# Kernel optimization log

Measured on AMD Instinct MI355X. Metric: run time of the kernel, lower is better.

The kernel has to match this reference:

```python
import jax, jax.numpy as jnp
import numpy as np

T, B, N, D, H = 128, 64, 24, 256, 8
F = D // H  # 32


def setup_inputs() -> dict:
    key = jax.random.key(0)
    ks = jax.random.split(key, 7)
    s = 1.0 / np.sqrt(D)  # torch nn.Linear default init range
    inputs = jax.random.normal(ks[0], (T, B, N * D), dtype=jnp.float32)
    Wk = jax.random.uniform(ks[1], (H, F, D), minval=-s, maxval=s, dtype=jnp.float32)
    bk = jax.random.uniform(ks[2], (H, F), minval=-s, maxval=s, dtype=jnp.float32)
    Wv = jax.random.uniform(ks[3], (H, F, D), minval=-s, maxval=s, dtype=jnp.float32)
    bv = jax.random.uniform(ks[4], (H, F), minval=-s, maxval=s, dtype=jnp.float32)
    Wq = jax.random.uniform(ks[5], (H, N, F, D), minval=-s, maxval=s, dtype=jnp.float32)
    bq = jax.random.uniform(ks[6], (H, N, F), minval=-s, maxval=s, dtype=jnp.float32)
    return {"inputs": inputs, "Wk": Wk, "bk": bk, "Wv": Wv, "bv": bv, "Wq": Wq, "bq": bq}


def reference(inputs, Wk, bk, Wv, bv, Wq, bq):
    # inputs: (T, B, N*D) -> (T, B, N, D)
    x = inputs.reshape(T, B, N, D)
    # shared K/V per head: (T, B, H, N, F)
    k = jnp.einsum('tbnd,hfd->tbhnf', x, Wk) + bk[:, None, :]
    v = jnp.einsum('tbnd,hfd->tbhnf', x, Wv) + bv[:, None, :]
    # per-joint Q: joint n uses its own (F, D) weight -> (T, B, H, N, F)
    q = jnp.einsum('tbnd,hnfd->tbhnf', x, Wq) + bq
    # attention over joints, scaled by sqrt(F)
    scores = jnp.einsum('tbhnf,tbhmf->tbhnm', q, k) / jnp.sqrt(jnp.float32(F))
    attn = jax.nn.softmax(scores, axis=-1)
    out = jnp.einsum('tbhnm,tbhmf->tbhnf', attn, v)
    # concat heads along feature dim per joint, then flatten joints: (T, B, N*H*F)
    out = out.transpose(0, 1, 3, 2, 4).reshape(T, B, N * H * F)
    # dropout is identity in eval mode
    return out
```

## Files before the change

### kernel.cpp

```cpp
#include <hip/hip_runtime.h>
#include <hip/hip_bf16.h>
#include <cstdio>

#define TB  8192
#define N_  24
#define D_  256
#define H_  8
#define F_  32
#define ND  6144
#define HNF 6144

typedef unsigned short u16;
typedef __attribute__((ext_vector_type(8))) _Float16 f16x8;
typedef __attribute__((ext_vector_type(8))) short bf16x8;
typedef __attribute__((ext_vector_type(4))) float f32x4;

__device__ __forceinline__ u16 f2b(float f) {
    unsigned int u = __float_as_uint(f);
    return (u16)((u + 0x7FFFu + ((u >> 16) & 1u)) >> 16);
}
__device__ __forceinline__ float b2f(u16 s) {
    return __uint_as_float(((unsigned int)s) << 16);
}
__device__ __forceinline__ u16 f2h(float f) {
    _Float16 h = (_Float16)f;
    u16 u; __builtin_memcpy(&u, &h, 2); return u;
}

__device__ __forceinline__ void gl_lds16(const void* g, void* l) {
    __builtin_amdgcn_global_load_lds(
        (const __attribute__((address_space(1))) unsigned int*)g,
        (__attribute__((address_space(3))) unsigned int*)l, 16, 0, 0);
}

__global__ __launch_bounds__(256) void prep_weights(
    const float* __restrict__ Wk, const float* __restrict__ Wv,
    const float* __restrict__ Wq, u16* __restrict__ Bp)
{
    const int idx = blockIdx.x * 256 + threadIdx.x;
    if (idx >= 24 * 8 * 48 * 64) return;
    const int fr = idx & 15;
    const int fq = (idx >> 4) & 3;
    const int g  = (idx >> 6) % 48;
    const int kt = (idx / (64 * 48)) % 8;
    const int n  = idx / (64 * 48 * 8);
    const int col = g * 16 + fr;
    const int d0  = kt * 32 + fq * 8;
    const int c   = col & 255;
    const float* src;
    if (col < 256)      src = Wk + (size_t)c * 256 + d0;
    else if (col < 512) src = Wv + (size_t)c * 256 + d0;
    else {
        const int h = c >> 5, f = c & 31;
        src = Wq + ((size_t)(h * 24 + n) * 32 + f) * 256 + d0;
    }
    __align__(16) u16 out[8];
    #pragma unroll
    for (int j = 0; j < 8; ++j) out[j] = f2h(src[j]);
    *reinterpret_cast<uint4*>(Bp + (size_t)idx * 8) =
        *reinterpret_cast<const uint4*>(out);
}

__global__ __launch_bounds__(256) void prep_bias(
    const float* __restrict__ bk, const float* __restrict__ bv,
    const float* __restrict__ bq, float* __restrict__ biasp)
{
    const int idx = blockIdx.x * 256 + threadIdx.x;
    if (idx >= 24 * 768) return;
    const int col = idx % 768, n = idx / 768;
    const int c = col & 255;
    float v;
    if (col < 256)      v = bk[c];
    else if (col < 512) v = bv[c];
    else { const int h = c >> 5, f = c & 31; v = bq[(h * 24 + n) * 32 + f]; }
    biasp[n * 768 + col] = v;
}

__global__ __launch_bounds__(512, 4) void proj_mfma(
    const float* __restrict__ x,
    const u16* __restrict__ Bp,
    const float* __restrict__ biasp,
    u16* __restrict__ kb, u16* __restrict__ vb, u16* __restrict__ qb)
{
    const int lin  = blockIdx.x;
    const int mblk = lin & 63;
    const int ct   = (lin >> 6) % 3;
    const int n    = lin / 192;
    const int tb0  = mblk * 128;
    const int tid  = threadIdx.x;
    const int w    = tid >> 6;
    const int lane = tid & 63;
    const int wm   = w >> 2;
    const int wn   = w & 3;
    const int fr   = lane & 15, fq = lane >> 4;

    __shared__ __align__(16) u16 smem[32768];
    char* const Ab = (char*)smem;
    char* const Bb = (char*)smem + 16384;

    const int arow = tid >> 2;
    const int ac   = tid & 3;
    const float* xsrc = x + (size_t)(tb0 + arow) * ND + n * 256 + ac * 8;
    const int awbyte = arow * 64 + ((ac ^ ((arow >> 1) & 3)) << 4);

    const size_t bbase = (size_t)(n * 8 * 48 + ct * 16 + w * 2) * 1024 + lane * 16;

    f32x4 acc[4][4];
    #pragma unroll
    for (int m = 0; m < 4; ++m)
        #pragma unroll
        for (int j = 0; j < 4; ++j) acc[m][j] = (f32x4){0.f, 0.f, 0.f, 0.f};

    float4 axr[2][2];

    axr[0][0] = *reinterpret_cast<const float4*>(xsrc);
    axr[0][1] = *reinterpret_cast<const float4*>(xsrc + 4);
    gl_lds16((const char*)Bp + bbase,        Bb + (w * 2) * 1024);
    gl_lds16((const char*)Bp + bbase + 1024, Bb + (w * 2 + 1) * 1024);
    asm volatile("s_waitcnt vmcnt(2)" ::: "memory");
    {
        ushort4 hv;
        hv.x = f2h(axr[0][0].x); hv.y = f2h(axr[0][0].y);
        hv.z = f2h(axr[0][0].z); hv.w = f2h(axr[0][0].w);
        ushort4 hv2;
        hv2.x = f2h(axr[0][1].x); hv2.y = f2h(axr[0][1].y);
        hv2.z = f2h(axr[0][1].z); hv2.w = f2h(axr[0][1].w);
        *reinterpret_cast<ushort4*>(Ab + awbyte)     = hv;
        *reinterpret_cast<ushort4*>(Ab + awbyte + 8) = hv2;
    }
    axr[1][0] = *reinterpret_cast<const float4*>(xsrc + 32);
    axr[1][1] = *reinterpret_cast<const float4*>(xsrc + 36);
    asm volatile("s_waitcnt lgkmcnt(0)" ::: "memory");
    asm volatile("s_waitcnt vmcnt(2)" ::: "memory");
    __builtin_amdgcn_s_barrier();
    asm volatile("" ::: "memory");

    #pragma unroll
    for (int kt = 0; kt < 8; ++kt) {
        const int c = kt & 1, o = c ^ 1;

        if (kt < 7) {
            const size_t bs = bbase + (size_t)(kt + 1) * 48 * 1024;
            gl_lds16((const char*)Bp + bs,        Bb + o * 16384 + (w * 2) * 1024);
            gl_lds16((const char*)Bp + bs + 1024, Bb + o * 16384 + (w * 2 + 1) * 1024);
        }

        f16x8 bfr[4], afr[4];
        #pragma unroll
        for (int j = 0; j < 4; ++j)
            bfr[j] = *reinterpret_cast<const f16x8*>(
                Bb + c * 16384 + (wn * 4 + j) * 1024 + lane * 16);
        #pragma unroll
        for (int m = 0; m < 4; ++m) {
            const int row = wm * 64 + m * 16 + fr;
            afr[m] = *reinterpret_cast<const f16x8*>(
                Ab + c * 8192 + row * 64 + ((fq ^ ((fr >> 1) & 3)) << 4));
        }
        __builtin_amdgcn_s_setprio(1);
        #pragma unroll
        for (int j = 0; j < 4; ++j)
            #pragma unroll
            for (int m = 0; m < 4; ++m)
                acc[m][j] = __builtin_amdgcn_mfma_f32_16x16x32_f16(
                    afr[m], bfr[j], acc[m][j], 0, 0, 0);
        __builtin_amdgcn_s_setprio(0);

        if (kt < 7) {
            asm volatile("s_waitcnt vmcnt(2)" ::: "memory");
            __builtin_amdgcn_sched_barrier(0);
            {
                const float4 lo = axr[(kt + 1) & 1][0];
                const float4 hi = axr[(kt + 1) & 1][1];
                ushort4 hv;
                hv.x = f2h(lo.x); hv.y = f2h(lo.y); hv.z = f2h(lo.z); hv.w = f2h(lo.w);
                ushort4 hv2;
                hv2.x = f2h(hi.x); hv2.y = f2h(hi.y); hv2.z = f2h(hi.z); hv2.w = f2h(hi.w);
                *reinterpret_cast<ushort4*>(Ab + o * 8192 + awbyte)     = hv;
                *reinterpret_cast<ushort4*>(Ab + o * 8192 + awbyte + 8) = hv2;
            }
            if (kt < 6) {
                axr[kt & 1][0] = *reinterpret_cast<const float4*>(xsrc + (kt + 2) * 32);
                axr[kt & 1][1] = *reinterpret_cast<const float4*>(xsrc + (kt + 2) * 32 + 4);
            }
            asm volatile("s_waitcnt lgkmcnt(0)" ::: "memory");
            if (kt < 6) {
                asm volatile("s_waitcnt vmcnt(2)" ::: "memory");
            } else {
                asm volatile("s_waitcnt vmcnt(0)" ::: "memory");
            }
            __builtin_amdgcn_s_barrier();
            asm volatile("" ::: "memory");
        }
    }
    __syncthreads();

    #pragma unroll
    for (int j = 0; j < 4; ++j) {
        const int colL = wn * 64 + j * 16 + fr;
        const float bs = biasp[n * 768 + ct * 256 + colL];
        #pragma unroll
        for (int m = 0; m < 4; ++m)
            #pragma unroll
            for (int r = 0; r < 4; ++r) {
                const int rowL = wm * 64 + m * 16 + fq * 4 + r;
                const int byte = (rowL * 512 + colL * 2) ^ ((rowL & 7) << 4);
                *reinterpret_cast<u16*>((char*)smem + byte) = f2b(acc[m][j][r] + bs);
            }
    }
    __syncthreads();

    u16* dst = (ct == 0) ? kb : (ct == 1) ? vb : qb;
    #pragma unroll
    for (int it = 0; it < 8; ++it) {
        const int id  = it * 512 + tid;
        const int row = id >> 5;
        const int cch = id & 31;
        const uint4 v = *reinterpret_cast<const uint4*>(
            (char*)smem + (row * 512 + ((cch * 16) ^ ((row & 7) << 4))));
        const int cc = cch * 8;
        const int h  = cc >> 5, f0 = cc & 31;
        *reinterpret_cast<uint4*>(
            &dst[(size_t)(tb0 + row) * HNF + h * 768 + n * 32 + f0]) = v;
    }
}

__device__ __forceinline__ int swz(int row, int chunk) {
    return row * 32 + (((chunk ^ ((row >> 1) ^ (row >> 3))) & 3) << 3);
}

__global__ __launch_bounds__(256) void attn_mfma(
    const u16* __restrict__ kb,
    const u16* __restrict__ vb,
    const u16* __restrict__ qb,
    float* __restrict__ out)
{
    const int tid  = threadIdx.x;
    const int wid  = tid >> 6;
    const int lane = tid & 63;
    const int fr   = lane & 15;
    const int fq   = lane >> 4;
    const size_t tb = (size_t)blockIdx.x * 4 + wid;

    __shared__ __align__(16) u16 lds[4][2048];
    u16* Pw = lds[wid];
    u16* Vt = lds[wid] + 1024;

    #pragma unroll
    for (int i = 0; i < 4; ++i)
        reinterpret_cast<uint4*>(lds[wid])[lane + i * 64] = (uint4){0, 0, 0, 0};

    const u16* qt = qb + tb * HNF;
    const u16* kt = kb + tb * HNF;
    const u16* vt = vb + tb * HNF;
    float* outp = out + tb * ND;

    const float scale = 0.17677669529663687f;
    const bool colok = fr < 8;

    for (int h = 0; h < H_; ++h) {
        const u16* qh = qt + h * 768;
        const u16* kh = kt + h * 768;
        const u16* vh = vt + h * 768;

        bf16x8 qa[2], ka[2];
        #pragma unroll
        for (int t = 0; t < 2; ++t) {
            int rq = t * 16 + fr; rq = rq < 24 ? rq : 23;
            qa[t] = *reinterpret_cast<const bf16x8*>(qh + rq * 32 + fq * 8);
            ka[t] = *reinterpret_cast<const bf16x8*>(kh + rq * 32 + fq * 8);
        }

        {
            const int m = lane >> 2, q = lane & 3;
            const uint4 vv = *reinterpret_cast<const uint4*>(vh + m * 32 + q * 8);
            #pragma unroll
            for (int j = 0; j < 8; ++j) {
                const int f = q * 8 + j;
                Vt[swz(f, m >> 3) + (m & 7)] = reinterpret_cast<const u16*>(&vv)[j];
            }
            if (lane < 32) {
                const int m2 = 16 + (lane >> 2), q2 = lane & 3;
                const uint4 v2 = *reinterpret_cast<const uint4*>(vh + m2 * 32 + q2 * 8);
                #pragma unroll
                for (int j = 0; j < 8; ++j) {
                    const int f = q2 * 8 + j;
                    Vt[swz(f, m2 >> 3) + (m2 & 7)] = reinterpret_cast<const u16*>(&v2)[j];
                }
            }
        }

        f32x4 S[2][2];
        #pragma unroll
        for (int a = 0; a < 2; ++a)
            #pragma unroll
            for (int b = 0; b < 2; ++b)
                S[a][b] = __builtin_amdgcn_mfma_f32_16x16x32_bf16(
                    qa[a], ka[b], (f32x4){0.f, 0.f, 0.f, 0.f}, 0, 0, 0);

        float inv[2][4];
        #pragma unroll
        for (int t = 0; t < 2; ++t) {
            float e0[4], e1[4];
            #pragma unroll
            for (int r = 0; r < 4; ++r) {
                const float a = S[t][0][r] * scale;
                const float b = colok ? S[t][1][r] * scale : -1e30f;
                float mx = fmaxf(a, b);
                #pragma unroll
                for (int off = 1; off < 16; off <<= 1)
                    mx = fmaxf(mx, __shfl_xor(mx, off));
                e0[r] = __expf(a - mx);
                e1[r] = colok ? __expf(b - mx) : 0.f;
                float sm = e0[r] + e1[r];
                #pragma unroll
                for (int off = 1; off < 16; off <<= 1)
                    sm += __shfl_xor(sm, off);
                inv[t][r] = 1.f / sm;
            }
            #pragma unroll
            for (int r = 0; r < 4; ++r) {
                const int row = t * 16 + fq * 4 + r;
                if (row < 24) {
                    Pw[swz(row, fr >> 3) + (fr & 7)] = f2b(e0[r]);
                    if (colok) {
                        const int c1 = 16 + fr;
                        Pw[swz(row, c1 >> 3) + (c1 & 7)] = f2b(e1[r]);
                    }
                }
            }
        }

        bf16x8 pa[2], vbf[2];
        #pragma unroll
        for (int t = 0; t < 2; ++t)
            pa[t] = *reinterpret_cast<const bf16x8*>(&Pw[swz(t * 16 + fr, fq)]);
        #pragma unroll
        for (int t = 0; t < 2; ++t)
            vbf[t] = *reinterpret_cast<const bf16x8*>(&Vt[swz(t * 16 + fr, fq)]);

        f32x4 O[2][2];
        #pragma unroll
        for (int a = 0; a < 2; ++a)
            #pragma unroll
            for (int b = 0; b < 2; ++b)
                O[a][b] = __builtin_amdgcn_mfma_f32_16x16x32_bf16(
                    pa[a], vbf[b], (f32x4){0.f, 0.f, 0.f, 0.f}, 0, 0, 0);

        #pragma unroll
        for (int a = 0; a < 2; ++a)
            #pragma unroll
            for (int r = 0; r < 4; ++r) {
                const int row = a * 16 + fq * 4 + r;
                if (row < 24) {
                    outp[row * D_ + h * F_ + fr]      = O[a][0][r] * inv[a][r];
                    outp[row * D_ + h * F_ + 16 + fr] = O[a][1][r] * inv[a][r];
                }
            }
    }
}

extern "C" void kernel_launch(void* const* d_in, const int* in_sizes, int n_in,
                              void* d_out, int out_size, void* d_ws, size_t ws_size,
                              hipStream_t stream) {
    const float* x  = (const float*)d_in[0];
    const float* Wk = (const float*)d_in[1];
    const float* bk = (const float*)d_in[2];
    const float* Wv = (const float*)d_in[3];
    const float* bv = (const float*)d_in[4];
    const float* Wq = (const float*)d_in[5];
    const float* bq = (const float*)d_in[6];
    float* out = (float*)d_out;

    const size_t qkv_elems = (size_t)TB * HNF;
    const size_t need = qkv_elems * 2ull * 3ull;
    if (ws_size < need) fprintf(stderr, "ws too small: %zu < %zu\n", ws_size, need);
    u16* kbuf = (u16*)d_ws;
    u16* vbuf = kbuf + qkv_elems;
    u16* qbuf = vbuf + qkv_elems;

    u16*   Bp    = (u16*)d_out;
    float* biasp = (float*)((char*)d_out + (size_t)24 * 8 * 48 * 512 * 2);

    prep_weights<<<2304, 256, 0, stream>>>(Wk, Wv, Wq, Bp);
    prep_bias<<<(24 * 768 + 255) / 256, 256, 0, stream>>>(bk, bv, bq, biasp);
    proj_mfma<<<4608, 512, 0, stream>>>(x, Bp, biasp, kbuf, vbuf, qbuf);
    attn_mfma<<<TB / 4, 256, 0, stream>>>(kbuf, vbuf, qbuf, out);
}
```

Before: 322.1 us.

## Make projection blocks persistent over four M tiles with chunked epilogue

The projection kernel now runs a quarter as many blocks, and each loops over four 128-row M tiles, so the pipelined K loop runs continuously across tiles. Block indices are remapped so blocks sharing a joint's weights are grouped. The epilogue goes through a separate 16KB LDS region in 32-row chunks so it does not clobber the operand buffers, and bias values are loaded once into registers. The aim is to cut per-block launch and prologue cost and improve weight reuse. In exchange LDS grows to 64KB per block, which may lower occupancy, and the epilogue adds extra barriers.

```diff
diff --git a/kernel.cpp b/kernel.cpp
--- a/kernel.cpp
+++ b/kernel.cpp
@@ -82,145 +82,164 @@
     const float* __restrict__ biasp,
     u16* __restrict__ kb, u16* __restrict__ vb, u16* __restrict__ qb)
 {
-    const int lin  = blockIdx.x;
-    const int mblk = lin & 63;
-    const int ct   = (lin >> 6) % 3;
-    const int n    = lin / 192;
-    const int tb0  = mblk * 128;
-    const int tid  = threadIdx.x;
-    const int w    = tid >> 6;
+    const int b   = blockIdx.x;
+    const int grp = (b & 7) * 9 + ((b >> 3) % 9);
+    const int mch = b / 72;
+    const int n   = grp / 3;
+    const int ct  = grp % 3;
+    const int tid = threadIdx.x;
+    const int w   = tid >> 6;
     const int lane = tid & 63;
-    const int wm   = w >> 2;
-    const int wn   = w & 3;
-    const int fr   = lane & 15, fq = lane >> 4;
-
-    __shared__ __align__(16) u16 smem[32768];
-    char* const Ab = (char*)smem;
-    char* const Bb = (char*)smem + 16384;
+    const int wm  = w >> 2, wn = w & 3;
+    const int fr  = lane & 15, fq = lane >> 4;
+
+    __shared__ __align__(16) char smem[65536];
+    char* const Ab = smem;
+    char* const Bb = smem + 16384;
+    char* const Eb = smem + 49152;
 
     const int arow = tid >> 2;
     const int ac   = tid & 3;
-    const float* xsrc = x + (size_t)(tb0 + arow) * ND + n * 256 + ac * 8;
+    const float* xsrc0 = x + ((size_t)(mch * 512) + arow) * ND + n * 256 + ac * 8;
     const int awbyte = arow * 64 + ((ac ^ ((arow >> 1) & 3)) << 4);
 
-    const size_t bbase = (size_t)(n * 8 * 48 + ct * 16 + w * 2) * 1024 + lane * 16;
+    const char* Bpc = (const char*)Bp +
+        (size_t)(n * 8 * 48 + ct * 16 + w * 2) * 1024 + (size_t)lane * 16;
+
+    float biasv[4];
+    #pragma unroll
+    for (int j = 0; j < 4; ++j)
+        biasv[j] = biasp[n * 768 + ct * 256 + wn * 64 + j * 16 + fr];
 
     f32x4 acc[4][4];
-    #pragma unroll
-    for (int m = 0; m < 4; ++m)
-        #pragma unroll
-        for (int j = 0; j < 4; ++j) acc[m][j] = (f32x4){0.f, 0.f, 0.f, 0.f};
-
     float4 axr[2][2];
-
-    axr[0][0] = *reinterpret_cast<const float4*>(xsrc);
-    axr[0][1] = *reinterpret_cast<const float4*>(xsrc + 4);
-    gl_lds16((const char*)Bp + bbase,        Bb + (w * 2) * 1024);
-    gl_lds16((const char*)Bp + bbase + 1024, Bb + (w * 2 + 1) * 1024);
-    asm volatile("s_waitcnt vmcnt(2)" ::: "memory");
+    u16* dst = (ct == 0) ? kb : (ct == 1) ? vb : qb;
+
+    axr[0][0] = *reinterpret_cast<const float4*>(xsrc0);
+    axr[0][1] = *reinterpret_cast<const float4*>(xsrc0 + 4);
+    gl_lds16(Bpc,        Bb + (w * 2) * 1024);
+    gl_lds16(Bpc + 1024, Bb + (w * 2 + 1) * 1024);
     {
-        ushort4 hv;
-        hv.x = f2h(axr[0][0].x); hv.y = f2h(axr[0][0].y);
-        hv.z = f2h(axr[0][0].z); hv.w = f2h(axr[0][0].w);
-        ushort4 hv2;
+        ushort4 hv, hv2;
+        hv.x  = f2h(axr[0][0].x); hv.y  = f2h(axr[0][0].y);
+        hv.z  = f2h(axr[0][0].z); hv.w  = f2h(axr[0][0].w);
         hv2.x = f2h(axr[0][1].x); hv2.y = f2h(axr[0][1].y);
         hv2.z = f2h(axr[0][1].z); hv2.w = f2h(axr[0][1].w);
         *reinterpret_cast<ushort4*>(Ab + awbyte)     = hv;
         *reinterpret_cast<ushort4*>(Ab + awbyte + 8) = hv2;
     }
-    axr[1][0] = *reinterpret_cast<const float4*>(xsrc + 32);
-    axr[1][1] = *reinterpret_cast<const float4*>(xsrc + 36);
+    axr[1][0] = *reinterpret_cast<const float4*>(xsrc0 + 32);
+    axr[1][1] = *reinterpret_cast<const float4*>(xsrc0 + 36);
     asm volatile("s_waitcnt lgkmcnt(0)" ::: "memory");
     asm volatile("s_waitcnt vmcnt(2)" ::: "memory");
     __builtin_amdgcn_s_barrier();
     asm volatile("" ::: "memory");
 
     #pragma unroll
-    for (int kt = 0; kt < 8; ++kt) {
-        const int c = kt & 1, o = c ^ 1;
-
-        if (kt < 7) {
-            const size_t bs = bbase + (size_t)(kt + 1) * 48 * 1024;
-            gl_lds16((const char*)Bp + bs,        Bb + o * 16384 + (w * 2) * 1024);
-            gl_lds16((const char*)Bp + bs + 1024, Bb + o * 16384 + (w * 2 + 1) * 1024);
+    for (int mt = 0; mt < 4; ++mt) {
+        #pragma unroll
+        for (int m = 0; m < 4; ++m)
+            #pragma unroll
+            for (int j = 0; j < 4; ++j) acc[m][j] = (f32x4){0.f, 0.f, 0.f, 0.f};
+
+        #pragma unroll
+        for (int kt = 0; kt < 8; ++kt) {
+            const int i  = mt * 8 + kt;
+            const int cb = kt & 1, ob = cb ^ 1;
+
+            if (i < 31) {
+                const char* bs = Bpc + (size_t)((kt + 1) & 7) * 49152;
+                gl_lds16(bs,        Bb + ob * 16384 + (w * 2) * 1024);
+                gl_lds16(bs + 1024, Bb + ob * 16384 + (w * 2 + 1) * 1024);
+            }
+
+            f16x8 bfr[4], afr[4];
+            #pragma unroll
+            for (int j = 0; j < 4; ++j)
+                bfr[j] = *reinterpret_cast<const f16x8*>(
+                    Bb + cb * 16384 + (wn * 4 + j) * 1024 + lane * 16);
+            #pragma unroll
+            for (int m = 0; m < 4; ++m) {
+                const int row = wm * 64 + m * 16 + fr;
+                afr[m] = *reinterpret_cast<const f16x8*>(
+                    Ab + cb * 8192 + row * 64 + ((fq ^ ((fr >> 1) & 3)) << 4));
+            }
+            __builtin_amdgcn_s_setprio(1);
+            #pragma unroll
+            for (int j = 0; j < 4; ++j)
+                #pragma unroll
+                for (int m = 0; m < 4; ++m)
+                    acc[m][j] = __builtin_amdgcn_mfma_f32_16x16x32_f16(
+                        afr[m], bfr[j], acc[m][j], 0, 0, 0);
+            __builtin_amdgcn_s_setprio(0);
+
+            if (i < 31) {
+                const float4 lo = axr[(i + 1) & 1][0];
+                const float4 hi = axr[(i + 1) & 1][1];
+                ushort4 hv, hv2;
+                hv.x  = f2h(lo.x); hv.y  = f2h(lo.y); hv.z  = f2h(lo.z); hv.w  = f2h(lo.w);
+                hv2.x = f2h(hi.x); hv2.y = f2h(hi.y); hv2.z = f2h(hi.z); hv2.w = f2h(hi.w);
+                *reinterpret_cast<ushort4*>(Ab + ob * 8192 + awbyte)     = hv;
+                *reinterpret_cast<ushort4*>(Ab + ob * 8192 + awbyte + 8) = hv2;
+            }
+            if (i < 30) {
+                const int i2 = i + 2;
+                const float* p = xsrc0 + (size_t)(i2 >> 3) * (128 * ND) + (i2 & 7) * 32;
+                axr[i & 1][0] = *reinterpret_cast<const float4*>(p);
+                axr[i & 1][1] = *reinterpret_cast<const float4*>(p + 4);
+            }
+            if (i < 31) {
+                asm volatile("s_waitcnt lgkmcnt(0)" ::: "memory");
+                if (i < 30) { asm volatile("s_waitcnt vmcnt(2)" ::: "memory"); }
+                else        { asm volatile("s_waitcnt vmcnt(0)" ::: "memory"); }
+                __builtin_amdgcn_s_barrier();
+                asm volatile("" ::: "memory");
+            } else {
+                asm volatile("s_waitcnt lgkmcnt(0)" ::: "memory");
+                __builtin_amdgcn_s_barrier();
+                asm volatile("" ::: "memory");
+            }
         }
 
-        f16x8 bfr[4], afr[4];
-        #pragma unroll
-        for (int j = 0; j < 4; ++j)
-            bfr[j] = *reinterpret_cast<const f16x8*>(
-                Bb + c * 16384 + (wn * 4 + j) * 1024 + lane * 16);
-        #pragma unroll
-        for (int m = 0; m < 4; ++m) {
-            const int row = wm * 64 + m * 16 + fr;
-            afr[m] = *reinterpret_cast<const f16x8*>(
-                Ab + c * 8192 + row * 64 + ((fq ^ ((fr >> 1) & 3)) << 4));
-        }
-        __builtin_amdgcn_s_setprio(1);
-        #pragma unroll
-        for (int j = 0; j < 4; ++j)
-            #pragma unroll
-            for (int m = 0; m < 4; ++m)
-                acc[m][j] = __builtin_amdgcn_mfma_f32_16x16x32_f16(
-                    afr[m], bfr[j], acc[m][j], 0, 0, 0);
-        __builtin_amdgcn_s_setprio(0);
-
-        if (kt < 7) {
-            asm volatile("s_waitcnt vmcnt(2)" ::: "memory");
-            __builtin_amdgcn_sched_barrier(0);
-            {
-                const float4 lo = axr[(kt + 1) & 1][0];
-                const float4 hi = axr[(kt + 1) & 1][1];
-                ushort4 hv;
-                hv.x = f2h(lo.x); hv.y = f2h(lo.y); hv.z = f2h(lo.z); hv.w = f2h(lo.w);
-                ushort4 hv2;
-                hv2.x = f2h(hi.x); hv2.y = f2h(hi.y); hv2.z = f2h(hi.z); hv2.w = f2h(hi.w);
-                *reinterpret_cast<ushort4*>(Ab + o * 8192 + awbyte)     = hv;
-                *reinterpret_cast<ushort4*>(Ab + o * 8192 + awbyte + 8) = hv2;
-            }
-            if (kt < 6) {
-                axr[kt & 1][0] = *reinterpret_cast<const float4*>(xsrc + (kt + 2) * 32);
-                axr[kt & 1][1] = *reinterpret_cast<const float4*>(xsrc + (kt + 2) * 32 + 4);
+        const int tb0 = (mch * 4 + mt) * 128;
+        #pragma unroll
+        for (int p = 0; p < 4; ++p) {
+            if (wm == (p >> 1)) {
+                #pragma unroll
+                for (int mm = 0; mm < 2; ++mm) {
+                    const int m = (p & 1) * 2 + mm;
+                    #pragma unroll
+                    for (int j = 0; j < 4; ++j) {
+                        #pragma unroll
+                        for (int r = 0; r < 4; ++r) {
+                            const int rowLl = mm * 16 + fq * 4 + r;
+                            const int colL  = wn * 64 + j * 16 + fr;
+                            *reinterpret_cast<u16*>(Eb + rowLl * 512 +
+                                ((colL * 2) ^ ((rowLl & 7) << 4))) =
+                                f2b(acc[m][j][r] + biasv[j]);
+                        }
+                    }
+                }
             }
             asm volatile("s_waitcnt lgkmcnt(0)" ::: "memory");
-            if (kt < 6) {
-                asm volatile("s_waitcnt vmcnt(2)" ::: "memory");
-            } else {
-                asm volatile("s_waitcnt vmcnt(0)" ::: "memory");
-            }
+            __builtin_amdgcn_s_barrier();
+            asm volatile("" ::: "memory");
+            #pragma unroll
+            for (int it = 0; it < 2; ++it) {
+                const int id  = it * 512 + tid;
+                const int row = id >> 5;
+                const int cch = id & 31;
+                const uint4 v = *reinterpret_cast<const uint4*>(
+                    Eb + row * 512 + ((cch * 16) ^ ((row & 7) << 4)));
+                const int cc = cch * 8;
+                const int h  = cc >> 5, f0 = cc & 31;
+                *reinterpret_cast<uint4*>(
+                    &dst[(size_t)(tb0 + p * 32 + row) * HNF + h * 768 + n * 32 + f0]) = v;
+            }
+            asm volatile("s_waitcnt lgkmcnt(0)" ::: "memory");
             __builtin_amdgcn_s_barrier();
             asm volatile("" ::: "memory");
         }
-    }
-    __syncthreads();
-
-    #pragma unroll
-    for (int j = 0; j < 4; ++j) {
-        const int colL = wn * 64 + j * 16 + fr;
-        const float bs = biasp[n * 768 + ct * 256 + colL];
-        #pragma unroll
-        for (int m = 0; m < 4; ++m)
-            #pragma unroll
-            for (int r = 0; r < 4; ++r) {
-                const int rowL = wm * 64 + m * 16 + fq * 4 + r;
-                const int byte = (rowL * 512 + colL * 2) ^ ((rowL & 7) << 4);
-                *reinterpret_cast<u16*>((char*)smem + byte) = f2b(acc[m][j][r] + bs);
-            }
-    }
-    __syncthreads();
-
-    u16* dst = (ct == 0) ? kb : (ct == 1) ? vb : qb;
-    #pragma unroll
-    for (int it = 0; it < 8; ++it) {
-        const int id  = it * 512 + tid;
-        const int row = id >> 5;
-        const int cch = id & 31;
-        const uint4 v = *reinterpret_cast<const uint4*>(
-            (char*)smem + (row * 512 + ((cch * 16) ^ ((row & 7) << 4))));
-        const int cc = cch * 8;
-        const int h  = cc >> 5, f0 = cc & 31;
-        *reinterpret_cast<uint4*>(
-            &dst[(size_t)(tb0 + row) * HNF + h * 768 + n * 32 + f0]) = v;
     }
 }
 
@@ -293,9 +312,9 @@
         #pragma unroll
         for (int a = 0; a < 2; ++a)
             #pragma unroll
-            for (int b = 0; b < 2; ++b)
-                S[a][b] = __builtin_amdgcn_mfma_f32_16x16x32_bf16(
-                    qa[a], ka[b], (f32x4){0.f, 0.f, 0.f, 0.f}, 0, 0, 0);
+            for (int bb = 0; bb < 2; ++bb)
+                S[a][bb] = __builtin_amdgcn_mfma_f32_16x16x32_bf16(
+                    qa[a], ka[bb], (f32x4){0.f, 0.f, 0.f, 0.f}, 0, 0, 0);
 
         float inv[2][4];
         #pragma unroll
@@ -304,13 +323,13 @@
             #pragma unroll
             for (int r = 0; r < 4; ++r) {
                 const float a = S[t][0][r] * scale;
-                const float b = colok ? S[t][1][r] * scale : -1e30f;
-                float mx = fmaxf(a, b);
+                const float bbv = colok ? S[t][1][r] * scale : -1e30f;
+                float mx = fmaxf(a, bbv);
                 #pragma unroll
                 for (int off = 1; off < 16; off <<= 1)
                     mx = fmaxf(mx, __shfl_xor(mx, off));
                 e0[r] = __expf(a - mx);
-                e1[r] = colok ? __expf(b - mx) : 0.f;
+                e1[r] = colok ? __expf(bbv - mx) : 0.f;
                 float sm = e0[r] + e1[r];
                 #pragma unroll
                 for (int off = 1; off < 16; off <<= 1)
@@ -342,9 +361,9 @@
         #pragma unroll
         for (int a = 0; a < 2; ++a)
             #pragma unroll
-            for (int b = 0; b < 2; ++b)
-                O[a][b] = __builtin_amdgcn_mfma_f32_16x16x32_bf16(
-                    pa[a], vbf[b], (f32x4){0.f, 0.f, 0.f, 0.f}, 0, 0, 0);
+            for (int bb = 0; bb < 2; ++bb)
+                O[a][bb] = __builtin_amdgcn_mfma_f32_16x16x32_bf16(
+                    pa[a], vbf[bb], (f32x4){0.f, 0.f, 0.f, 0.f}, 0, 0, 0);
 
         #pragma unroll
         for (int a = 0; a < 2; ++a)
@@ -383,6 +402,6 @@
 
     prep_weights<<<2304, 256, 0, stream>>>(Wk, Wv, Wq, Bp);
     prep_bias<<<(24 * 768 + 255) / 256, 256, 0, stream>>>(bk, bv, bq, biasp);
-    proj_mfma<<<4608, 512, 0, stream>>>(x, Bp, biasp, kbuf, vbuf, qbuf);
+    proj_mfma<<<1152, 512, 0, stream>>>(x, Bp, biasp, kbuf, vbuf, qbuf);
     attn_mfma<<<TB / 4, 256, 0, stream>>>(kbuf, vbuf, qbuf, out);
 }
```

Result: slower. 430.4 us (+33.6%).
